# Kernel optimization log

Measured on AMD Instinct MI355X. Metric: run time of the kernel, lower is better.

The kernel has to match this reference:

```python
import jax, jax.numpy as jnp
import numpy as np

INPUT_DIM = 256
NODE_DIM = 6
OUTPUT_DIM = 256
N_NODES = 10000
N_EDGES = 320000


def setup_inputs() -> dict:
    key = jax.random.key(0)
    ks = jax.random.split(key, 6)
    x = jax.random.normal(ks[0], (N_NODES, NODE_DIM), dtype=jnp.float32)
    edge_index = jax.random.randint(ks[1], (2, N_EDGES), 0, N_NODES, dtype=jnp.int64 if jax.config.jax_enable_x64 else jnp.int32)
    edge_attr = jax.random.normal(ks[2], (N_EDGES, INPUT_DIM), dtype=jnp.float32)
    mask = jax.random.uniform(ks[3], (N_EDGES,), dtype=jnp.float32)
    in_feat = INPUT_DIM * 3 + NODE_DIM * 2  # 774
    limit = float(np.sqrt(6.0 / (in_feat + OUTPUT_DIM)))  # xavier_uniform
    W = jax.random.uniform(ks[4], (OUTPUT_DIM, in_feat), dtype=jnp.float32, minval=-limit, maxval=limit)
    b = jax.random.uniform(ks[5], (OUTPUT_DIM,), dtype=jnp.float32, minval=-1.0 / np.sqrt(in_feat), maxval=1.0 / np.sqrt(in_feat))
    return {"x": x, "num_nodes": N_NODES, "edge_index": edge_index, "edge_attr": edge_attr, "mask": mask, "W": W, "b": b}


def reference(x, num_nodes, edge_index, edge_attr, mask, W, b):
    row = edge_index[0]
    col = edge_index[1]
    # masked mean-ish aggregation of edge features into destination nodes
    num = jax.ops.segment_sum(edge_attr * mask[:, None], col, num_segments=num_nodes)  # [N, input_dim]
    den = jax.ops.segment_sum(mask[:, None], col, num_segments=num_nodes)             # [N, 1]
    node_rep = num / (den + 1.0)
    node_rep = jnp.concatenate([node_rep, x], axis=1)  # [N, input_dim + node_dim]
    edge_rep = jnp.concatenate([node_rep[row], node_rep[col], edge_attr], axis=-1)  # [E, 3*input_dim + 2*node_dim]
    edge_rep = edge_rep @ W.T + b  # [E, output_dim]
    return (node_rep, edge_rep)
```

## Files before the change

kernel.cpp:

```cpp
#include <hip/hip_runtime.h>
#include <hip/hip_bf16.h>
#include <stdint.h>

typedef __attribute__((ext_vector_type(4))) float f32x4;
typedef __attribute__((ext_vector_type(8))) short bf16x8;

#define NDIM 6
#define IN_DIM 256
#define OUT_DIM 256
#define KW 780
#define NR 262
#define NRP 320
#define SCAN_T 1024

__device__ __forceinline__ short f2bf(float f) {
  return __builtin_bit_cast(short, __float2bfloat16(f));
}
__device__ __forceinline__ float bf2f(short h) {
  unsigned int u = ((unsigned int)(unsigned short)h) << 16;
  return __builtin_bit_cast(float, u);
}

__device__ __forceinline__ void gload_lds16(void* lds, const void* g) {
  __builtin_amdgcn_global_load_lds(
      (const __attribute__((address_space(1))) unsigned int*)g,
      (__attribute__((address_space(3))) unsigned int*)lds, 16, 0, 0);
}

__global__ void hist_kernel(const int* __restrict__ ei, int* __restrict__ counts, int E) {
  int e = blockIdx.x * 256 + threadIdx.x;
  if (e < E) atomicAdd(&counts[ei[(long)E + e]], 1);
}

__global__ __launch_bounds__(SCAN_T) void scan_kernel(const int* __restrict__ counts,
                                                      int* __restrict__ offsets, int N) {
  __shared__ int part[SCAN_T];
  int t = threadIdx.x;
  int chunk = (N + SCAN_T - 1) / SCAN_T;
  int begin = t * chunk;
  int s = 0;
  for (int i = 0; i < chunk; ++i) {
    int idx = begin + i;
    if (idx < N) s += counts[idx];
  }
  part[t] = s;
  __syncthreads();
  for (int d = 1; d < SCAN_T; d <<= 1) {
    int v = (t >= d) ? part[t - d] : 0;
    __syncthreads();
    part[t] += v;
    __syncthreads();
  }
  int run = (t == 0) ? 0 : part[t - 1];
  for (int i = 0; i < chunk; ++i) {
    int idx = begin + i;
    if (idx < N) { offsets[idx] = run; run += counts[idx]; }
  }
}

__global__ void scatter_kernel(const int* __restrict__ ei, const int* __restrict__ offsets,
                               int* __restrict__ cursor, int* __restrict__ csr, int E) {
  int e = blockIdx.x * 256 + threadIdx.x;
  if (e >= E) return;
  int col = ei[(long)E + e];
  int pos = atomicAdd(&cursor[col], 1);
  csr[offsets[col] + pos] = e;
}

__global__ __launch_bounds__(256) void reduce_kernel(
    const int* __restrict__ csr, const int* __restrict__ offsets,
    const int* __restrict__ counts, const float* __restrict__ ea,
    const float* __restrict__ mask, const float* __restrict__ x,
    float* __restrict__ outN, short* __restrict__ nrepb, int N) {
  int n = blockIdx.x * 4 + (threadIdx.x >> 6);
  if (n >= N) return;
  int lane = threadIdx.x & 63;
  int s = offsets[n], cnt = counts[n];
  f32x4 sum = (f32x4)0.0f;
  float den = 0.0f;

  int ecur = 0; float mcur = 0.0f;
  if (lane < cnt) { ecur = csr[s + lane]; mcur = mask[ecur]; }

  for (int base = 0; base < cnt; base += 64) {
    int enext = 0; float mnext = 0.0f;
    if (base + 64 < cnt) {
      int idx = base + 64 + lane;
      if (idx < cnt) { enext = csr[s + idx]; mnext = mask[enext]; }
    }
    int mbits = __builtin_bit_cast(int, mcur);
#pragma unroll
    for (int i = 0; i < 64; ++i) {
      if (base + i >= cnt) break;
      int e = __builtin_amdgcn_readlane(ecur, i);
      float m = __builtin_bit_cast(float, __builtin_amdgcn_readlane(mbits, i));
      f32x4 v = ((const f32x4*)ea)[(long)e * 64 + lane];
      sum.x += v.x * m; sum.y += v.y * m; sum.z += v.z * m; sum.w += v.w * m;
      den += m;
    }
    ecur = enext; mcur = mnext;
  }

  float inv = 1.0f / (den + 1.0f);
  sum.x *= inv; sum.y *= inv; sum.z *= inv; sum.w *= inv;
  float* po = outN + (long)n * NR + lane * 4;
  po[0] = sum.x; po[1] = sum.y; po[2] = sum.z; po[3] = sum.w;
  short4 pb;
  pb.x = f2bf(sum.x); pb.y = f2bf(sum.y); pb.z = f2bf(sum.z); pb.w = f2bf(sum.w);
  *(short4*)(nrepb + (long)n * NRP + lane * 4) = pb;
  if (lane < NDIM) {
    float xv = x[(long)n * NDIM + lane];
    outN[(long)n * NR + IN_DIM + lane] = xv;
    nrepb[(long)n * NRP + IN_DIM + lane] = f2bf(xv);
  } else if (lane < 8) {
    nrepb[(long)n * NRP + IN_DIM + lane] = 0;
  }
}

__global__ void wprep_kernel(const float* __restrict__ W, short* __restrict__ Weat,
                             short* __restrict__ Wrt, short* __restrict__ Wct) {
  int idx = blockIdx.x * 256 + threadIdx.x;
  if (idx < OUT_DIM * 256) {
    int n = idx >> 8, k = idx & 255;
    Weat[idx] = f2bf(W[(long)n * KW + 2 * NR + k]);
    return;
  }
  idx -= OUT_DIM * 256;
  if (idx < OUT_DIM * NRP) {
    int n = idx / NRP, k = idx % NRP;
    Wrt[idx] = f2bf(k < NR ? W[(long)n * KW + k] : 0.0f);
    return;
  }
  idx -= OUT_DIM * NRP;
  if (idx < OUT_DIM * NRP) {
    int n = idx / NRP, k = idx % NRP;
    Wct[idx] = f2bf(k < NR ? W[(long)n * KW + NR + k] : 0.0f);
  }
}

__global__ __launch_bounds__(256, 2) void pgemm_kernel(
    const short* __restrict__ nrepb, const short* __restrict__ Wrt,
    const short* __restrict__ Wct, const float* __restrict__ bias,
    short* __restrict__ Pr, short* __restrict__ Pc, int N) {
  __shared__ short As[5][64 * 64];
  const int tid = threadIdx.x;
  const int wave = tid >> 6, lane = tid & 63;
  const int m0 = blockIdx.x * 64;
  const int table = blockIdx.y;
  const short* Wt = table ? Wct : Wrt;
  short* P = table ? Pc : Pr;
  const int nbase = wave * 64;

  float bvals[4];
#pragma unroll
  for (int nf = 0; nf < 4; ++nf)
    bvals[nf] = table ? 0.0f : bias[nbase + 16 * nf + (lane & 15)];

  f32x4 acc[4][4];
#pragma unroll
  for (int mf = 0; mf < 4; ++mf)
#pragma unroll
    for (int nf = 0; nf < 4; ++nf) acc[mf][nf] = (f32x4)0.0f;

  bf16x8 bv[2][8];
  auto loadB = [&](int t, int tb) {
#pragma unroll
    for (int s2 = 0; s2 < 2; ++s2)
#pragma unroll
      for (int nf = 0; nf < 4; ++nf)
        bv[tb][s2 * 4 + nf] = *(const bf16x8*)&Wt[
            (long)(nbase + nf * 16 + (lane & 15)) * NRP + t * 64 + s2 * 32 + (lane >> 4) * 8];
  };

  const int scp = lane & 7;
#pragma unroll
  for (int t = 0; t < 5; ++t)
#pragma unroll
    for (int i = 0; i < 2; ++i) {
      int row = 16 * wave + 8 * i + (lane >> 3);
      int c = scp ^ (row & 7);
      long m = m0 + row; if (m >= N) m = N - 1;
      gload_lds16(&As[t][(16 * wave + 8 * i) * 64], nrepb + m * NRP + t * 64 + 8 * c);
    }
  loadB(0, 0);
  asm volatile("s_waitcnt vmcnt(8)" ::: "memory");
  __builtin_amdgcn_s_barrier();
  __builtin_amdgcn_sched_barrier(0);

#pragma unroll
  for (int t = 0; t < 5; ++t) {
    if (t < 4) loadB(t + 1, (t + 1) & 1);
    if (t < 4) asm volatile("s_waitcnt vmcnt(8)" ::: "memory");
    else       asm volatile("s_waitcnt vmcnt(0)" ::: "memory");
#pragma unroll
    for (int s2 = 0; s2 < 2; ++s2) {
      bf16x8 a[4];
      int cl = s2 * 4 + (lane >> 4);
#pragma unroll
      for (int mf = 0; mf < 4; ++mf) {
        int m = 16 * mf + (lane & 15);
        a[mf] = *(const bf16x8*)&As[t][m * 64 + ((cl ^ (m & 7)) * 8)];
      }
#pragma unroll
      for (int mf = 0; mf < 4; ++mf)
#pragma unroll
        for (int nf = 0; nf < 4; ++nf)
          acc[mf][nf] = __builtin_amdgcn_mfma_f32_16x16x32_bf16(
              a[mf], bv[t & 1][s2 * 4 + nf], acc[mf][nf], 0, 0, 0);
    }
  }

#pragma unroll
  for (int mf = 0; mf < 4; ++mf)
#pragma unroll
    for (int nf = 0; nf < 4; ++nf)
#pragma unroll
      for (int q = 0; q < 4; ++q) {
        long m = m0 + 16 * mf + (lane >> 4) * 4 + q;
        if (m < N)
          P[m * OUT_DIM + nbase + 16 * nf + (lane & 15)] = f2bf(acc[mf][nf][q] + bvals[nf]);
      }
}

__global__ __launch_bounds__(256, 3) void egemm_kernel(
    const int* __restrict__ ei, const float* __restrict__ ea,
    const short* __restrict__ Weat, const short* __restrict__ Pr,
    const short* __restrict__ Pc, float* __restrict__ outE, int E) {
  __shared__ float Abuf[2][64 * 64];
  const int tid = threadIdx.x;
  const int wave = tid >> 6, lane = tid & 63;
  const long e0 = (long)blockIdx.x * 64;
  const int l15 = lane & 15, lg = lane >> 4;
  const int nbase = wave * 64;

  f32x4 acc[4][4];
#pragma unroll
  for (int mf = 0; mf < 4; ++mf)
#pragma unroll
    for (int nf = 0; nf < 4; ++nf) acc[mf][nf] = (f32x4)0.0f;

  const short* brow[4];
#pragma unroll
  for (int nf = 0; nf < 4; ++nf)
    brow[nf] = Weat + (nbase + 16 * nf + l15) * 256 + lg * 8;

  bf16x8 bks[2][4];
  auto loadBks = [&](int ks, int kb) {
#pragma unroll
    for (int nf = 0; nf < 4; ++nf)
      bks[kb][nf] = *(const bf16x8*)(brow[nf] + ks * 32);
  };

  auto stageA = [&](int t, int buf) {
#pragma unroll
    for (int j = 0; j < 4; ++j) {
      int c = j * 256 + tid;
      int r = c >> 4, pp = c & 15;
      long e = e0 + r; if (e >= E) e = E - 1;
      const float* src = ea + e * IN_DIM + t * 64 + ((pp ^ (r & 15)) << 2);
      gload_lds16(&Abuf[buf][(j * 256 + wave * 64) << 2], src);
    }
  };

  auto computeKs = [&](int ks, int kb) {
    const int buf = (ks >> 1) & 1, ks2 = ks & 1;
    bf16x8 a[4];
#pragma unroll
    for (int mf = 0; mf < 4; ++mf) {
      int r = 16 * mf + l15;
      int q0 = ks2 * 8 + lg * 2;
      f32x4 v0 = *(const f32x4*)&Abuf[buf][(r * 16 + (q0 ^ (r & 15))) << 2];
      f32x4 v1 = *(const f32x4*)&Abuf[buf][(r * 16 + ((q0 + 1) ^ (r & 15))) << 2];
      bf16x8 p;
      p[0] = f2bf(v0.x); p[1] = f2bf(v0.y); p[2] = f2bf(v0.z); p[3] = f2bf(v0.w);
      p[4] = f2bf(v1.x); p[5] = f2bf(v1.y); p[6] = f2bf(v1.z); p[7] = f2bf(v1.w);
      a[mf] = p;
    }
    __builtin_amdgcn_s_setprio(1);
#pragma unroll
    for (int mf = 0; mf < 4; ++mf)
#pragma unroll
      for (int nf = 0; nf < 4; ++nf)
        acc[mf][nf] = __builtin_amdgcn_mfma_f32_16x16x32_bf16(
            a[mf], bks[kb][nf], acc[mf][nf], 0, 0, 0);
    __builtin_amdgcn_s_setprio(0);
  };

  stageA(0, 0);
  loadBks(0, 0);
  asm volatile("s_waitcnt vmcnt(4)" ::: "memory");
  __builtin_amdgcn_s_barrier();
  __builtin_amdgcn_sched_barrier(0);

#pragma unroll
  for (int t = 0; t < 4; ++t) {
    loadBks(2 * t + 1, 1);
    if (t < 3) stageA(t + 1, (t + 1) & 1);
    if (t < 3) asm volatile("s_waitcnt vmcnt(8)" ::: "memory");
    else       asm volatile("s_waitcnt vmcnt(4)" ::: "memory");
    __builtin_amdgcn_sched_barrier(0);
    computeKs(2 * t, 0);
    if (t < 3) loadBks(2 * t + 2, 0);
    if (t < 3) asm volatile("s_waitcnt vmcnt(8)" ::: "memory");
    else       asm volatile("s_waitcnt vmcnt(0)" ::: "memory");
    __builtin_amdgcn_sched_barrier(0);
    computeKs(2 * t + 1, 1);
    if (t < 3) {
      asm volatile("s_waitcnt vmcnt(4)" ::: "memory");
      __builtin_amdgcn_s_barrier();
      __builtin_amdgcn_sched_barrier(0);
    }
  }

#pragma unroll
  for (int mf = 0; mf < 4; ++mf) {
#pragma unroll
    for (int q = 0; q < 4; ++q) {
      long e = e0 + 16 * mf + lg * 4 + q;
      bool ok = e < E;
      long ec = ok ? e : (E - 1);
      int re = ei[ec], ce = ei[(long)E + ec];
      const short* pr = Pr + (long)re * OUT_DIM;
      const short* pc = Pc + (long)ce * OUT_DIM;
      if (ok) {
#pragma unroll
        for (int nf = 0; nf < 4; ++nf) {
          int n = nbase + 16 * nf + l15;
          outE[e * OUT_DIM + n] = acc[mf][nf][q] + bf2f(pr[n]) + bf2f(pc[n]);
        }
      }
    }
  }
}

extern "C" void kernel_launch(void* const* d_in, const int* in_sizes, int n_in,
                              void* d_out, int out_size, void* d_ws, size_t ws_size,
                              hipStream_t stream) {
  const float* x    = (const float*)d_in[0];
  const int*   ei   = (const int*)d_in[2];
  const float* ea   = (const float*)d_in[3];
  const float* mask = (const float*)d_in[4];
  const float* W    = (const float*)d_in[5];
  const float* b    = (const float*)d_in[6];
  const int E = in_sizes[4];
  const int N = in_sizes[0] / NDIM;

  char* p = (char*)d_ws;
  int* counts  = (int*)p; p += (long)N * 4;
  int* cursor  = (int*)p; p += (long)N * 4;
  int* offsets = (int*)p; p += (long)(N + 1) * 4;
  int* csr     = (int*)p; p += (long)E * 4;
  p = (char*)(((uintptr_t)p + 15) & ~(uintptr_t)15);
  short* nrepb = (short*)p; p += (long)N * NRP * 2;
  short* Weat  = (short*)p; p += (long)OUT_DIM * 256 * 2;
  short* Wrt   = (short*)p; p += (long)OUT_DIM * NRP * 2;
  short* Wct   = (short*)p; p += (long)OUT_DIM * NRP * 2;
  short* Pr    = (short*)p; p += (long)N * OUT_DIM * 2;
  short* Pc    = (short*)p;

  float* outN = (float*)d_out;
  float* outE = outN + (long)N * NR;

  hipMemsetAsync(counts, 0, (size_t)2 * N * 4, stream);

  hist_kernel<<<(E + 255) / 256, 256, 0, stream>>>(ei, counts, E);
  scan_kernel<<<1, SCAN_T, 0, stream>>>(counts, offsets, N);
  scatter_kernel<<<(E + 255) / 256, 256, 0, stream>>>(ei, offsets, cursor, csr, E);
  reduce_kernel<<<(N + 3) / 4, 256, 0, stream>>>(csr, offsets, counts, ea, mask, x,
                                                 outN, nrepb, N);
  int wtot = OUT_DIM * 256 + 2 * OUT_DIM * NRP;
  wprep_kernel<<<(wtot + 255) / 256, 256, 0, stream>>>(W, Weat, Wrt, Wct);
  dim3 pg((N + 63) / 64, 2);
  pgemm_kernel<<<pg, 256, 0, stream>>>(nrepb, Wrt, Wct, b, Pr, Pc, N);
  egemm_kernel<<<(E + 63) / 64, 256, 0, stream>>>(ei, ea, Weat, Pr, Pc, outE, E);
}
```

Before: 395.6 us.

## Emit bf16 edge_attr copy during reduce and feed bf16 edge GEMM

The node-reduce kernel already reads every fp32 edge_attr row, so it now also writes a bf16 copy into workspace. A new edge GEMM kernel loads that bf16 copy straight into LDS, whole K at once with an XOR swizzle, instead of reading and converting fp32 data. The aim is to halve the bytes the edge GEMM reads. The cost is an extra scattered 2-byte-per-element write in the reduce kernel, so total traffic may end up roughly the same. The new path is only taken if the workspace is large enough, otherwise the old fp32 kernel runs.

```diff
diff --git a/kernel.cpp b/kernel.cpp
--- a/kernel.cpp
+++ b/kernel.cpp
@@ -71,7 +71,8 @@
     const int* __restrict__ csr, const int* __restrict__ offsets,
     const int* __restrict__ counts, const float* __restrict__ ea,
     const float* __restrict__ mask, const float* __restrict__ x,
-    float* __restrict__ outN, short* __restrict__ nrepb, int N) {
+    float* __restrict__ outN, short* __restrict__ nrepb,
+    short* __restrict__ eab, int N) {
   int n = blockIdx.x * 4 + (threadIdx.x >> 6);
   if (n >= N) return;
   int lane = threadIdx.x & 63;
@@ -95,6 +96,11 @@
       int e = __builtin_amdgcn_readlane(ecur, i);
       float m = __builtin_bit_cast(float, __builtin_amdgcn_readlane(mbits, i));
       f32x4 v = ((const f32x4*)ea)[(long)e * 64 + lane];
+      if (eab) {
+        short4 vb;
+        vb.x = f2bf(v.x); vb.y = f2bf(v.y); vb.z = f2bf(v.z); vb.w = f2bf(v.w);
+        *(short4*)(eab + (long)e * IN_DIM + lane * 4) = vb;
+      }
       sum.x += v.x * m; sum.y += v.y * m; sum.z += v.z * m; sum.w += v.w * m;
       den += m;
     }
@@ -222,7 +228,92 @@
       }
 }
 
-__global__ __launch_bounds__(256, 3) void egemm_kernel(
+__global__ __launch_bounds__(256, 3) void egemm_bf16(
+    const int* __restrict__ ei, const short* __restrict__ eab,
+    const short* __restrict__ Weat, const short* __restrict__ Pr,
+    const short* __restrict__ Pc, float* __restrict__ outE, int E) {
+  __shared__ short Abuf[64 * 256];
+  const int tid = threadIdx.x;
+  const int wave = tid >> 6, lane = tid & 63;
+  const long e0 = (long)blockIdx.x * 64;
+  const int l15 = lane & 15, lg = lane >> 4;
+  const int nbase = wave * 64;
+
+  f32x4 acc[4][4];
+#pragma unroll
+  for (int mf = 0; mf < 4; ++mf)
+#pragma unroll
+    for (int nf = 0; nf < 4; ++nf) acc[mf][nf] = (f32x4)0.0f;
+
+  const short* brow[4];
+#pragma unroll
+  for (int nf = 0; nf < 4; ++nf)
+    brow[nf] = Weat + (nbase + 16 * nf + l15) * 256 + lg * 8;
+
+  bf16x8 bks[2][4];
+  auto loadBks = [&](int ks, int kb) {
+#pragma unroll
+    for (int nf = 0; nf < 4; ++nf)
+      bks[kb][nf] = *(const bf16x8*)(brow[nf] + ks * 32);
+  };
+
+#pragma unroll
+  for (int j = 0; j < 8; ++j) {
+    int c8 = j * 256 + tid;
+    int r = c8 >> 5, pp = c8 & 31;
+    long e = e0 + r; if (e >= E) e = E - 1;
+    const short* src = eab + e * IN_DIM + ((pp ^ (r & 7)) << 3);
+    gload_lds16(&Abuf[(j * 256 + wave * 64) << 3], src);
+  }
+  loadBks(0, 0);
+  asm volatile("s_waitcnt vmcnt(4)" ::: "memory");
+  __builtin_amdgcn_s_barrier();
+  __builtin_amdgcn_sched_barrier(0);
+
+#pragma unroll
+  for (int ks = 0; ks < 8; ++ks) {
+    if (ks < 7) loadBks(ks + 1, (ks + 1) & 1);
+    if (ks < 7) asm volatile("s_waitcnt vmcnt(4)" ::: "memory");
+    else        asm volatile("s_waitcnt vmcnt(0)" ::: "memory");
+    __builtin_amdgcn_sched_barrier(0);
+    bf16x8 a[4];
+#pragma unroll
+    for (int mf = 0; mf < 4; ++mf) {
+      int r = 16 * mf + l15;
+      a[mf] = *(const bf16x8*)&Abuf[r * 256 + (((ks * 4 + lg) ^ (r & 7)) << 3)];
+    }
+    __builtin_amdgcn_s_setprio(1);
+#pragma unroll
+    for (int mf = 0; mf < 4; ++mf)
+#pragma unroll
+      for (int nf = 0; nf < 4; ++nf)
+        acc[mf][nf] = __builtin_amdgcn_mfma_f32_16x16x32_bf16(
+            a[mf], bks[ks & 1][nf], acc[mf][nf], 0, 0, 0);
+    __builtin_amdgcn_s_setprio(0);
+  }
+
+#pragma unroll
+  for (int mf = 0; mf < 4; ++mf) {
+#pragma unroll
+    for (int q = 0; q < 4; ++q) {
+      long e = e0 + 16 * mf + lg * 4 + q;
+      bool ok = e < E;
+      long ec = ok ? e : (E - 1);
+      int re = ei[ec], ce = ei[(long)E + ec];
+      const short* pr = Pr + (long)re * OUT_DIM;
+      const short* pc = Pc + (long)ce * OUT_DIM;
+      if (ok) {
+#pragma unroll
+        for (int nf = 0; nf < 4; ++nf) {
+          int n = nbase + 16 * nf + l15;
+          outE[e * OUT_DIM + n] = acc[mf][nf][q] + bf2f(pr[n]) + bf2f(pc[n]);
+        }
+      }
+    }
+  }
+}
+
+__global__ __launch_bounds__(256, 3) void egemm_f32(
     const int* __restrict__ ei, const float* __restrict__ ea,
     const short* __restrict__ Weat, const short* __restrict__ Pr,
     const short* __restrict__ Pc, float* __restrict__ outE, int E) {
@@ -356,7 +447,10 @@
   short* Wrt   = (short*)p; p += (long)OUT_DIM * NRP * 2;
   short* Wct   = (short*)p; p += (long)OUT_DIM * NRP * 2;
   short* Pr    = (short*)p; p += (long)N * OUT_DIM * 2;
-  short* Pc    = (short*)p;
+  short* Pc    = (short*)p; p += (long)N * OUT_DIM * 2;
+  p = (char*)(((uintptr_t)p + 15) & ~(uintptr_t)15);
+  short* eab   = (short*)p; p += (long)E * IN_DIM * 2;
+  bool use_eab = ((size_t)(p - (char*)d_ws) <= ws_size);
 
   float* outN = (float*)d_out;
   float* outE = outN + (long)N * NR;
@@ -367,10 +461,14 @@
   scan_kernel<<<1, SCAN_T, 0, stream>>>(counts, offsets, N);
   scatter_kernel<<<(E + 255) / 256, 256, 0, stream>>>(ei, offsets, cursor, csr, E);
   reduce_kernel<<<(N + 3) / 4, 256, 0, stream>>>(csr, offsets, counts, ea, mask, x,
-                                                 outN, nrepb, N);
+                                                 outN, nrepb,
+                                                 use_eab ? eab : (short*)nullptr, N);
   int wtot = OUT_DIM * 256 + 2 * OUT_DIM * NRP;
   wprep_kernel<<<(wtot + 255) / 256, 256, 0, stream>>>(W, Weat, Wrt, Wct);
   dim3 pg((N + 63) / 64, 2);
   pgemm_kernel<<<pg, 256, 0, stream>>>(nrepb, Wrt, Wct, b, Pr, Pc, N);
-  egemm_kernel<<<(E + 63) / 64, 256, 0, stream>>>(ei, ea, Weat, Pr, Pc, outE, E);
-}
+  if (use_eab)
+    egemm_bf16<<<(E + 63) / 64, 256, 0, stream>>>(ei, eab, Weat, Pr, Pc, outE, E);
+  else
+    egemm_f32<<<(E + 63) / 64, 256, 0, stream>>>(ei, ea, Weat, Pr, Pc, outE, E);
+}
```

Result: slower. 433.0 us (+9.5%).
